# Kernel optimization log

Measured on AMD Instinct MI355X. Metric: run time of the kernel, lower is better.

The kernel has to match this reference:

```python
import jax, jax.numpy as jnp
import numpy as np

L_LEVELS = 16
T_SIZE = 524288
F_DIM = 2
GROWTH = 1.38
N_PTS = 1048576


def setup_inputs() -> dict:
    key = jax.random.key(0)
    k1, k2 = jax.random.split(key)
    xy = jax.random.uniform(k1, (N_PTS, 2), dtype=jnp.float32, minval=-1.0, maxval=1.0)
    # flax nn.initializers.uniform(0.0001) -> U[0, 1e-4)
    tables = jax.random.uniform(k2, (L_LEVELS, T_SIZE, F_DIM), dtype=jnp.float32) * 1e-4
    return {"xy": xy, "tables": tables}


def reference(xy, tables):
    PI1 = jnp.int32(-1640531535)
    PI2 = jnp.int32(805459861)
    L, T, F = tables.shape
    N = xy.shape[0]
    # static per-level resolutions: res_l = int(16 * b**l)
    res = jnp.asarray([int(16 * GROWTH ** l) for l in range(L)], dtype=jnp.float32)  # (L,)
    sc = (xy * 0.5 + 0.5)[None, :, :] * res[:, None, None]        # (L, N, 2)
    fl = jnp.floor(sc).astype(jnp.int32)                          # (L, N, 2)
    fr = sc - fl.astype(jnp.float32)                              # (L, N, 2)
    offsets = jnp.array([[0, 0], [1, 0], [0, 1], [1, 1]], dtype=jnp.int32)  # (4, 2)
    corners = fl[:, :, None, :] + offsets                         # (L, N, 4, 2)
    cx = corners[..., 0]
    cy = corners[..., 1]
    # int32 wraparound multiply + xor, mod table size, abs (matches source)
    h = jnp.abs(jnp.mod(jnp.bitwise_xor(cx * PI1, cy * PI2), T))  # (L, N, 4)
    # per-level gather of 4 corner embeddings
    cf = jax.vmap(lambda t, idx: t[idx])(tables, h)               # (L, N, 4, F)
    fx = fr[..., 0:1]                                             # (L, N, 1)
    fy = fr[..., 1:2]
    w = jnp.stack([(1 - fx) * (1 - fy), fx * (1 - fy), (1 - fx) * fy, fx * fy], axis=2)  # (L, N, 4, 1)
    out = jnp.sum(w * cf, axis=2)                                 # (L, N, F)
    # concat levels along feature dim, level-major order as in source
    return jnp.moveaxis(out, 0, 1).reshape(N, L * F)              # (N, L*F)
```

## Files before the change

kernel.cpp:

```cpp
#include <hip/hip_runtime.h>
#include <cstdint>

#define T_MASK 0x7FFFFu
#define PI1 0x9E3779B1u
#define PI2 805459861u
#define NPTS 1048576

typedef float floatx4 __attribute__((ext_vector_type(4)));
typedef float floatx2 __attribute__((ext_vector_type(2)));

__device__ __forceinline__ floatx2 corner_blend(const float* __restrict__ tb,
                                                float u, float v, float res) {
    const float sx = u * res, sy = v * res;
    const float flx = floorf(sx), fly = floorf(sy);
    const float fx = sx - flx, fy = sy - fly;
    const uint32_t hx0 = (uint32_t)(int)flx * PI1, hx1 = hx0 + PI1;
    const uint32_t hy0 = (uint32_t)(int)fly * PI2, hy1 = hy0 + PI2;
    const floatx2* __restrict__ t2 = (const floatx2*)tb;
    const floatx2 c00 = t2[(hx0 ^ hy0) & T_MASK];
    const floatx2 c10 = t2[(hx1 ^ hy0) & T_MASK];
    const floatx2 c01 = t2[(hx0 ^ hy1) & T_MASK];
    const floatx2 c11 = t2[(hx1 ^ hy1) & T_MASK];
    const float w00 = (1.f - fx) * (1.f - fy), w10 = fx * (1.f - fy);
    const float w01 = (1.f - fx) * fy,         w11 = fx * fy;
    floatx2 r;
    r.x = w00 * c00.x + w10 * c10.x + w01 * c01.x + w11 * c11.x;
    r.y = w00 * c00.y + w10 * c10.y + w01 * c01.y + w11 * c11.y;
    return r;
}

__global__ __launch_bounds__(256) void k_heavy(const float* __restrict__ xy,
                                               const float* __restrict__ tables,
                                               float* __restrict__ ws) {
    const float resH[4] = {763.f, 1053.f, 1453.f, 2005.f};
    const uint32_t b = blockIdx.x;
    const uint32_t xcd = b & 7u;
    const uint32_t li = xcd & 3u;
    const uint32_t half = xcd >> 2;
    const uint32_t c = b >> 3u;
    const uint32_t p0 = half * (NPTS / 2u) + c * 512u + threadIdx.x * 2u;

    const floatx4 pxy = __builtin_nontemporal_load(
        (const floatx4*)(xy + 2ull * p0));
    const float* __restrict__ tb = tables + (size_t)(12u + li) * 1048576u;
    const float res = resH[li];

    const floatx2 r0 = corner_blend(tb, pxy.x * 0.5f + 0.5f, pxy.y * 0.5f + 0.5f, res);
    const floatx2 r1 = corner_blend(tb, pxy.z * 0.5f + 0.5f, pxy.w * 0.5f + 0.5f, res);
    floatx4 o;
    o.x = r0.x; o.y = r0.y; o.z = r1.x; o.w = r1.y;
    __builtin_nontemporal_store(o,
        (floatx4*)(ws + (size_t)li * (2u * NPTS) + 2ull * p0));
}

__global__ __launch_bounds__(256) void k_light(const float* __restrict__ xy,
                                               const float* __restrict__ tables,
                                               const float* __restrict__ ws,
                                               float* __restrict__ out) {
    __shared__ float sm[4 * 2048];
    const float resL[12] = {16.f, 22.f, 30.f, 42.f, 58.f, 80.f, 110.f, 152.f,
                            210.f, 290.f, 400.f, 553.f};
    const uint32_t n = blockIdx.x * 256u + threadIdx.x;

    const floatx2 p = __builtin_nontemporal_load((const floatx2*)(xy + 2ull * n));
    const float u = p.x * 0.5f + 0.5f, v = p.y * 0.5f + 0.5f;

    float o[32];
#pragma unroll
    for (int l = 0; l < 12; ++l) {
        const floatx2 r = corner_blend(tables + (size_t)l * 1048576u, u, v, resL[l]);
        o[2 * l] = r.x; o[2 * l + 1] = r.y;
    }
#pragma unroll
    for (int li = 0; li < 4; ++li) {
        const floatx2 r = __builtin_nontemporal_load(
            (const floatx2*)(ws + (size_t)li * (2u * NPTS) + 2ull * n));
        o[24 + 2 * li] = r.x; o[25 + 2 * li] = r.y;
    }

    const uint32_t w = threadIdx.x >> 6, lane = threadIdx.x & 63u;
    float* ms = sm + w * 2048u;
#pragma unroll
    for (int j = 0; j < 8; ++j)
        *(floatx4*)(ms + lane * 32u + 4u * (j ^ (lane & 7u))) =
            *(const floatx4*)(o + 4 * j);
    __syncthreads();

    const size_t obase = ((size_t)blockIdx.x * 256u + w * 64u) * 32u;
#pragma unroll
    for (int k = 0; k < 8; ++k) {
        const uint32_t t = k * 8u + (lane >> 3);
        const uint32_t jc = (lane & 7u) ^ (t & 7u);
        const floatx4 vv = *(const floatx4*)(ms + t * 32u + 4u * jc);
        __builtin_nontemporal_store(vv,
            (floatx4*)(out + obase + (size_t)(k * 256u + lane * 4u)));
    }
}

__global__ __launch_bounds__(256) void k_fallback(const float* __restrict__ xy,
                                                  const float* __restrict__ tables,
                                                  float* __restrict__ out, int n_pts) {
    int n = blockIdx.x * 256 + threadIdx.x;
    if (n >= n_pts) return;
    const float2 p = *reinterpret_cast<const float2*>(xy + 2ull * n);
    const float u = p.x * 0.5f + 0.5f, v = p.y * 0.5f + 0.5f;
    const float res[16] = {16.f, 22.f, 30.f, 42.f, 58.f, 80.f, 110.f, 152.f,
                           210.f, 290.f, 400.f, 553.f, 763.f, 1053.f, 1453.f, 2005.f};
    float o[32];
#pragma unroll
    for (int l = 0; l < 16; ++l) {
        const floatx2 r = corner_blend(tables + (size_t)l * 1048576u, u, v, res[l]);
        o[2 * l] = r.x; o[2 * l + 1] = r.y;
    }
    floatx4* o4 = reinterpret_cast<floatx4*>(out + (size_t)n * 32u);
#pragma unroll
    for (int j = 0; j < 8; ++j) o4[j] = *(const floatx4*)(&o[4 * j]);
}

extern "C" void kernel_launch(void* const* d_in, const int* in_sizes, int n_in,
                              void* d_out, int out_size, void* d_ws, size_t ws_size,
                              hipStream_t stream) {
    const float* xy     = (const float*)d_in[0];
    const float* tables = (const float*)d_in[1];
    float* out          = (float*)d_out;
    const int n_pts = in_sizes[0] / 2;

    const size_t ws_need = 4ull * NPTS * 2ull * sizeof(float);
    if (n_pts == NPTS && ws_size >= ws_need) {
        float* ws = (float*)d_ws;
        k_heavy<<<8192, 256, 0, stream>>>(xy, tables, ws);
        k_light<<<NPTS / 256, 256, 0, stream>>>(xy, tables, ws, out);
    } else {
        k_fallback<<<(n_pts + 255) / 256, 256, 0, stream>>>(xy, tables, out, n_pts);
    }
}
```

Before: 574.0 us.

## Split hashed levels into per-level serial phase kernels before merge

Replaces the single heavy kernel, which spread the four finest levels across XCDs, with one kernel launch per level for levels 7 through 15. Each launch writes its blended features to a workspace slot, and a merge kernel computes the coarse levels directly and gathers the stored levels. The intent is to let each level's 4 MB table stay resident in cache during its own pass, reducing random-gather misses. The cost is more launches and extra workspace write and read traffic, and it falls back to a seven-phase variant when the workspace is smaller.

Result: faster. 481.9 us (-16.0%).

```diff
diff --git a/kernel.cpp b/kernel.cpp
--- a/kernel.cpp
+++ b/kernel.cpp
@@ -8,6 +8,12 @@
 
 typedef float floatx4 __attribute__((ext_vector_type(4)));
 typedef float floatx2 __attribute__((ext_vector_type(2)));
+
+__device__ __forceinline__ float res_of(int l) {
+    const float r[16] = {16.f, 22.f, 30.f, 42.f, 58.f, 80.f, 110.f, 152.f,
+                         210.f, 290.f, 400.f, 553.f, 763.f, 1053.f, 1453.f, 2005.f};
+    return r[l];
+}
 
 __device__ __forceinline__ floatx2 corner_blend(const float* __restrict__ tb,
                                                 float u, float v, float res) {
@@ -29,53 +35,39 @@
     return r;
 }
 
-__global__ __launch_bounds__(256) void k_heavy(const float* __restrict__ xy,
+template<int L, int SLOT>
+__global__ __launch_bounds__(256) void k_phase(const float* __restrict__ xy,
                                                const float* __restrict__ tables,
                                                float* __restrict__ ws) {
-    const float resH[4] = {763.f, 1053.f, 1453.f, 2005.f};
-    const uint32_t b = blockIdx.x;
-    const uint32_t xcd = b & 7u;
-    const uint32_t li = xcd & 3u;
-    const uint32_t half = xcd >> 2;
-    const uint32_t c = b >> 3u;
-    const uint32_t p0 = half * (NPTS / 2u) + c * 512u + threadIdx.x * 2u;
-
-    const floatx4 pxy = __builtin_nontemporal_load(
-        (const floatx4*)(xy + 2ull * p0));
-    const float* __restrict__ tb = tables + (size_t)(12u + li) * 1048576u;
-    const float res = resH[li];
-
-    const floatx2 r0 = corner_blend(tb, pxy.x * 0.5f + 0.5f, pxy.y * 0.5f + 0.5f, res);
-    const floatx2 r1 = corner_blend(tb, pxy.z * 0.5f + 0.5f, pxy.w * 0.5f + 0.5f, res);
-    floatx4 o;
-    o.x = r0.x; o.y = r0.y; o.z = r1.x; o.w = r1.y;
-    __builtin_nontemporal_store(o,
-        (floatx4*)(ws + (size_t)li * (2u * NPTS) + 2ull * p0));
+    const uint32_t n = blockIdx.x * 256u + threadIdx.x;
+    const floatx2 p = __builtin_nontemporal_load((const floatx2*)(xy + 2ull * n));
+    const floatx2 r = corner_blend(tables + (size_t)L * 1048576u,
+                                   p.x * 0.5f + 0.5f, p.y * 0.5f + 0.5f, res_of(L));
+    __builtin_nontemporal_store(r,
+        (floatx2*)(ws + (size_t)SLOT * 2097152u + 2ull * n));
 }
 
-__global__ __launch_bounds__(256) void k_light(const float* __restrict__ xy,
+template<int NIN, int NWS>
+__global__ __launch_bounds__(256) void k_merge(const float* __restrict__ xy,
                                                const float* __restrict__ tables,
                                                const float* __restrict__ ws,
                                                float* __restrict__ out) {
     __shared__ float sm[4 * 2048];
-    const float resL[12] = {16.f, 22.f, 30.f, 42.f, 58.f, 80.f, 110.f, 152.f,
-                            210.f, 290.f, 400.f, 553.f};
     const uint32_t n = blockIdx.x * 256u + threadIdx.x;
-
     const floatx2 p = __builtin_nontemporal_load((const floatx2*)(xy + 2ull * n));
     const float u = p.x * 0.5f + 0.5f, v = p.y * 0.5f + 0.5f;
 
     float o[32];
 #pragma unroll
-    for (int l = 0; l < 12; ++l) {
-        const floatx2 r = corner_blend(tables + (size_t)l * 1048576u, u, v, resL[l]);
+    for (int l = 0; l < NIN; ++l) {
+        const floatx2 r = corner_blend(tables + (size_t)l * 1048576u, u, v, res_of(l));
         o[2 * l] = r.x; o[2 * l + 1] = r.y;
     }
 #pragma unroll
-    for (int li = 0; li < 4; ++li) {
+    for (int s = 0; s < NWS; ++s) {
         const floatx2 r = __builtin_nontemporal_load(
-            (const floatx2*)(ws + (size_t)li * (2u * NPTS) + 2ull * n));
-        o[24 + 2 * li] = r.x; o[25 + 2 * li] = r.y;
+            (const floatx2*)(ws + (size_t)s * 2097152u + 2ull * n));
+        o[2 * (NIN + s)] = r.x; o[2 * (NIN + s) + 1] = r.y;
     }
 
     const uint32_t w = threadIdx.x >> 6, lane = threadIdx.x & 63u;
@@ -104,12 +96,10 @@
     if (n >= n_pts) return;
     const float2 p = *reinterpret_cast<const float2*>(xy + 2ull * n);
     const float u = p.x * 0.5f + 0.5f, v = p.y * 0.5f + 0.5f;
-    const float res[16] = {16.f, 22.f, 30.f, 42.f, 58.f, 80.f, 110.f, 152.f,
-                           210.f, 290.f, 400.f, 553.f, 763.f, 1053.f, 1453.f, 2005.f};
     float o[32];
 #pragma unroll
     for (int l = 0; l < 16; ++l) {
-        const floatx2 r = corner_blend(tables + (size_t)l * 1048576u, u, v, res[l]);
+        const floatx2 r = corner_blend(tables + (size_t)l * 1048576u, u, v, res_of(l));
         o[2 * l] = r.x; o[2 * l + 1] = r.y;
     }
     floatx4* o4 = reinterpret_cast<floatx4*>(out + (size_t)n * 32u);
@@ -125,11 +115,31 @@
     float* out          = (float*)d_out;
     const int n_pts = in_sizes[0] / 2;
 
-    const size_t ws_need = 4ull * NPTS * 2ull * sizeof(float);
-    if (n_pts == NPTS && ws_size >= ws_need) {
+    const size_t slot_bytes = 2097152ull * 4ull;
+    const int grid = NPTS / 256;
+
+    if (n_pts == NPTS && ws_size >= 9 * slot_bytes) {
         float* ws = (float*)d_ws;
-        k_heavy<<<8192, 256, 0, stream>>>(xy, tables, ws);
-        k_light<<<NPTS / 256, 256, 0, stream>>>(xy, tables, ws, out);
+        k_phase<15, 8><<<grid, 256, 0, stream>>>(xy, tables, ws);
+        k_phase<14, 7><<<grid, 256, 0, stream>>>(xy, tables, ws);
+        k_phase<13, 6><<<grid, 256, 0, stream>>>(xy, tables, ws);
+        k_phase<12, 5><<<grid, 256, 0, stream>>>(xy, tables, ws);
+        k_phase<11, 4><<<grid, 256, 0, stream>>>(xy, tables, ws);
+        k_phase<10, 3><<<grid, 256, 0, stream>>>(xy, tables, ws);
+        k_phase< 9, 2><<<grid, 256, 0, stream>>>(xy, tables, ws);
+        k_phase< 8, 1><<<grid, 256, 0, stream>>>(xy, tables, ws);
+        k_phase< 7, 0><<<grid, 256, 0, stream>>>(xy, tables, ws);
+        k_merge<7, 9><<<grid, 256, 0, stream>>>(xy, tables, ws, out);
+    } else if (n_pts == NPTS && ws_size >= 7 * slot_bytes) {
+        float* ws = (float*)d_ws;
+        k_phase<15, 6><<<grid, 256, 0, stream>>>(xy, tables, ws);
+        k_phase<14, 5><<<grid, 256, 0, stream>>>(xy, tables, ws);
+        k_phase<13, 4><<<grid, 256, 0, stream>>>(xy, tables, ws);
+        k_phase<12, 3><<<grid, 256, 0, stream>>>(xy, tables, ws);
+        k_phase<11, 2><<<grid, 256, 0, stream>>>(xy, tables, ws);
+        k_phase<10, 1><<<grid, 256, 0, stream>>>(xy, tables, ws);
+        k_phase< 9, 0><<<grid, 256, 0, stream>>>(xy, tables, ws);
+        k_merge<9, 7><<<grid, 256, 0, stream>>>(xy, tables, ws, out);
     } else {
         k_fallback<<<(n_pts + 255) / 256, 256, 0, stream>>>(xy, tables, out, n_pts);
     }
```
